# Optimization experiments

Measured on AMD Instinct MI355X. Metric: run time of the kernel, lower is better.

The kernel has to match this reference:

```python
import jax, jax.numpy as jnp
import numpy as np

N_A, N_B = 100000, 100000
N = N_A + N_B
E = 600000
D_IN_A, D_IN_B = 64, 96
HID, OUT = 128, 64
R, BASES = 4, 4


def setup_inputs() -> dict:
    key = jax.random.key(0)
    ks = jax.random.split(key, 16)
    inp = {
        "x_author": jax.random.normal(ks[0], (N_A, D_IN_A), jnp.float32),
        "x_paper": jax.random.normal(ks[1], (N_B, D_IN_B), jnp.float32),
        "src": jax.random.randint(ks[2], (E,), 0, N, jnp.int32),
        "dst": jax.random.randint(ks[3], (E,), 0, N, jnp.int32),
        "edge_type": jax.random.randint(ks[4], (E,), 0, R, jnp.int32),
        # per-node-type linear projections (with bias, as nn.Linear)
        "W_proj_a": jax.random.normal(ks[5], (D_IN_A, HID), jnp.float32) / np.sqrt(D_IN_A),
        "b_proj_a": jnp.zeros((HID,), jnp.float32),
        "W_proj_b": jax.random.normal(ks[6], (D_IN_B, HID), jnp.float32) / np.sqrt(D_IN_B),
        "b_proj_b": jnp.zeros((HID,), jnp.float32),
        # conv0: hid->hid, root_weight=False
        "basis0": jax.random.normal(ks[7], (BASES, HID, HID), jnp.float32) / np.sqrt(HID),
        "comp0": jax.random.normal(ks[8], (R, BASES), jnp.float32) / np.sqrt(BASES),
        # conv1: hid->hid, root_weight=True
        "basis1": jax.random.normal(ks[9], (BASES, HID, HID), jnp.float32) / np.sqrt(HID),
        "comp1": jax.random.normal(ks[10], (R, BASES), jnp.float32) / np.sqrt(BASES),
        "root1": jax.random.normal(ks[11], (HID, HID), jnp.float32) / np.sqrt(HID),
        # conv2: hid->out, root_weight=True
        "basis2": jax.random.normal(ks[12], (BASES, HID, OUT), jnp.float32) / np.sqrt(HID),
        "comp2": jax.random.normal(ks[13], (R, BASES), jnp.float32) / np.sqrt(BASES),
        "root2": jax.random.normal(ks[14], (HID, OUT), jnp.float32) / np.sqrt(HID),
    }
    return inp


def rgcn_conv(x, src, dst, etype, basis, comp, root):
    # basis-decomposed relation weights: [R, in, out]
    W = jnp.einsum('rb,bio->rio', comp, basis)
    out = jnp.zeros((x.shape[0], W.shape[2]), x.dtype)
    for r in range(R):  # small fixed relation count
        xw = x @ W[r]                                  # [N, out]
        m = (etype == r)
        msg = jnp.where(m[:, None], xw[src], 0.0)      # [E, out]
        s = jax.ops.segment_sum(msg, dst, num_segments=x.shape[0])
        cnt = jax.ops.segment_sum(m.astype(x.dtype), dst, num_segments=x.shape[0])
        out = out + s / jnp.maximum(cnt, 1.0)[:, None]  # per-relation mean aggr
    if root is not None:
        out = out + x @ root
    return out


def reference(x_author, x_paper, src, dst, edge_type,
              W_proj_a, b_proj_a, W_proj_b, b_proj_b,
              basis0, comp0, basis1, comp1, root1, basis2, comp2, root2):
    # per-node-type projection + relu, then concat in node_type order
    ha = jax.nn.relu(x_author @ W_proj_a + b_proj_a)
    hp = jax.nn.relu(x_paper @ W_proj_b + b_proj_b)
    x = jnp.concatenate([ha, hp], axis=0)             # [N, HID]
    x_lat0 = x
    # dropout skipped (eval mode)
    x = jax.nn.relu(rgcn_conv(x, src, dst, edge_type, basis0, comp0, None))
    x_lat1 = x
    x = jax.nn.relu(rgcn_conv(x, src, dst, edge_type, basis1, comp1, root1))
    x_lat2 = x
    x = rgcn_conv(x, src, dst, edge_type, basis2, comp2, root2)
    return (x, x_lat0, x_lat1, x_lat2)
```

## Files before the change

### kernel.cpp

```cpp
#include <hip/hip_runtime.h>

constexpr int NNODES = 200000;
constexpr int NAUT   = 100000;
constexpr int NEDGE  = 600000;
constexpr int HIDC   = 128;
constexpr int OUTCH  = 64;
constexpr int RELS   = 4;
constexpr int SCAN_N = RELS * NNODES;
constexpr int LDB    = HIDC + 8;

typedef __attribute__((ext_vector_type(8))) short bf16x8;
typedef __attribute__((ext_vector_type(4))) float f32x4;

__device__ __forceinline__ unsigned short f2bf(float f) {
    unsigned int b = __float_as_uint(f);
    b += 0x7FFFu + ((b >> 16) & 1u);
    return (unsigned short)(b >> 16);
}
__device__ __forceinline__ float bf2f(unsigned short u) {
    return __uint_as_float(((unsigned int)u) << 16);
}

__device__ __forceinline__ int fragoff(int k, int n, int NB) {
    return ((k >> 5) * NB + (n >> 4)) * 512 + (((k >> 3) & 3) * 16 + (n & 15)) * 8 + (k & 7);
}


__global__ void count_kernel(const int* __restrict__ dst, const int* __restrict__ et,
                             int* __restrict__ bins) {
    int e = blockIdx.x * 256 + threadIdx.x;
    if (e < NEDGE) atomicAdd(&bins[et[e] * NNODES + dst[e]], 1);
}

__global__ void scan_fused_kernel(int* __restrict__ bins, int* __restrict__ binCur,
                                  int* __restrict__ gctr) {
    __shared__ int s[256];
    __shared__ int sbase;
    int b = blockIdx.x, t = threadIdx.x;
    int base = b * 1024 + t * 4;
    int v[4], sum = 0;
#pragma unroll
    for (int i = 0; i < 4; i++) {
        v[i] = (base + i < SCAN_N) ? bins[base + i] : 0;
        sum += v[i];
    }
    s[t] = sum;
    __syncthreads();
    for (int off = 1; off < 256; off <<= 1) {
        int x = (t >= off) ? s[t - off] : 0;
        __syncthreads();
        if (t >= off) s[t] += x;
        __syncthreads();
    }
    if (t == 255) sbase = atomicAdd(gctr, s[255]);
    __syncthreads();
    int run = sbase + s[t] - sum;
#pragma unroll
    for (int i = 0; i < 4; i++) {
        if (base + i < SCAN_N) {
            bins[base + i] = run;
            binCur[base + i] = run;
        }
        run += v[i];
    }
}

__global__ void scatter_kernel(const int* __restrict__ src, const int* __restrict__ dst,
                               const int* __restrict__ et, int* __restrict__ binCur,
                               int* __restrict__ srcSorted) {
    int e = blockIdx.x * 256 + threadIdx.x;
    if (e < NEDGE) {
        int bin = et[e] * NNODES + dst[e];
        int pos = atomicAdd(&binCur[bin], 1);
        srcSorted[pos] = src[e];
    }
}

__global__ void fragify_kernel(const float* __restrict__ basis0, const float* __restrict__ comp0,
                               const float* __restrict__ basis1, const float* __restrict__ comp1,
                               const float* __restrict__ root1,
                               const float* __restrict__ basis2, const float* __restrict__ comp2,
                               const float* __restrict__ root2,
                               short* __restrict__ whi0, short* __restrict__ wlo0,
                               short* __restrict__ whi1, short* __restrict__ wlo1,
                               short* __restrict__ whiR1, short* __restrict__ wloR1,
                               short* __restrict__ whi2, short* __restrict__ wlo2,
                               short* __restrict__ whiR2, short* __restrict__ wloR2) {
    int idx = blockIdx.x * 256 + threadIdx.x;
    if (idx >= 188416) return;
    float w;
    short *hp, *lp;
    if (idx < 65536) {
        int r = idx >> 14, e = idx & 16383;
        int k = e >> 7, n = e & 127;
        w = 0.f;
#pragma unroll
        for (int b = 0; b < 4; b++) w += comp0[r * 4 + b] * basis0[b * 16384 + e];
        int off = r * 16384 + fragoff(k, n, 8);
        hp = whi0 + off; lp = wlo0 + off;
    } else if (idx < 131072) {
        int i2 = idx - 65536;
        int r = i2 >> 14, e = i2 & 16383;
        int k = e >> 7, n = e & 127;
        w = 0.f;
#pragma unroll
        for (int b = 0; b < 4; b++) w += comp1[r * 4 + b] * basis1[b * 16384 + e];
        int off = r * 16384 + fragoff(k, n, 8);
        hp = whi1 + off; lp = wlo1 + off;
    } else if (idx < 147456) {
        int e = idx - 131072;
        int k = e >> 7, n = e & 127;
        w = root1[e];
        int off = fragoff(k, n, 8);
        hp = whiR1 + off; lp = wloR1 + off;
    } else if (idx < 180224) {
        int i2 = idx - 147456;
        int r = i2 >> 13, e = i2 & 8191;
        int k = e >> 6, n = e & 63;
        w = 0.f;
#pragma unroll
        for (int b = 0; b < 4; b++) w += comp2[r * 4 + b] * basis2[b * 8192 + e];
        int off = r * 8192 + fragoff(k, n, 4);
        hp = whi2 + off; lp = wlo2 + off;
    } else {
        int e = idx - 180224;
        int k = e >> 6, n = e & 63;
        w = root2[e];
        int off = fragoff(k, n, 4);
        hp = whiR2 + off; lp = wloR2 + off;
    }
    unsigned short h = f2bf(w);
    unsigned short l = f2bf(w - bf2f(h));
    *hp = (short)h;
    *lp = (short)l;
}

__global__ __launch_bounds__(256) void gemm_kernel(const float* __restrict__ A,
                                                   const float* __restrict__ B,
                                                   const float* __restrict__ bias,
                                                   float* __restrict__ C, int M, int K) {
    __shared__ float sA[64 * 128];
    int tid = threadIdx.x;
    int row0 = blockIdx.x * 64;

    for (int i = tid; i < (64 * K) >> 2; i += 256) {
        int off = i << 2;
        int rr = off / K, cc = off % K;
        int row = row0 + rr;
        float4 v = {0.f, 0.f, 0.f, 0.f};
        if (row < M) v = *(const float4*)(A + (long)row * K + cc);
        *(float4*)(sA + rr * K + cc) = v;
    }
    __syncthreads();

    int cg = tid & 31, rg = tid >> 5;
    int c0 = cg * 4, r0 = rg * 8;
    float acc[8][4];
#pragma unroll
    for (int i = 0; i < 8; i++)
#pragma unroll
        for (int j = 0; j < 4; j++) acc[i][j] = 0.f;

#pragma unroll 2
    for (int k = 0; k < K; k += 4) {
        float a[8][4];
#pragma unroll
        for (int i = 0; i < 8; i++)
            *(float4*)(a[i]) = *(const float4*)(sA + (r0 + i) * K + k);
#pragma unroll
        for (int j = 0; j < 4; j++) {
            float b[4];
            *(float4*)b = *(const float4*)(B + (k + j) * 128 + c0);
#pragma unroll
            for (int i = 0; i < 8; i++)
#pragma unroll
                for (int jj = 0; jj < 4; jj++)
                    acc[i][jj] = fmaf(a[i][j], b[jj], acc[i][jj]);
        }
    }

#pragma unroll
    for (int i = 0; i < 8; i++) {
        int row = row0 + r0 + i;
        if (row >= M) continue;
        float v[4];
#pragma unroll
        for (int jj = 0; jj < 4; jj++) v[jj] = fmaxf(acc[i][jj] + bias[c0 + jj], 0.f);
        *(float4*)(C + (long)row * 128 + c0) = *(float4*)v;
    }
}

template <int NC, bool HASROOT, bool DORELU>
__global__ __launch_bounds__(512) void conv_kernel(const float* __restrict__ x,
                                                   const short* __restrict__ whiRel,
                                                   const short* __restrict__ wloRel,
                                                   const short* __restrict__ whiRoot,
                                                   const short* __restrict__ wloRoot,
                                                   const int* __restrict__ binStart,
                                                   const int* __restrict__ binEnd,
                                                   const int* __restrict__ srcSorted,
                                                   float* __restrict__ out) {
    constexpr int NB  = NC / 16;
    constexpr int KB  = HIDC / 32;
    constexpr int TPW = NB / 2;
    __shared__ short sHi[64 * LDB];
    __shared__ short sLo[64 * LDB];
    int tid = threadIdx.x;
    int v0 = blockIdx.x * 64;

    const int grow = tid >> 3, gq = tid & 7;
    const int wave = tid >> 6, lane = tid & 63;
    const int lrow = lane & 15, lgrp = lane >> 4;
    const int rt = wave >> 1, ch = wave & 1;

    f32x4 acc[TPW];
#pragma unroll
    for (int t = 0; t < TPW; t++) acc[t] = (f32x4){0.f, 0.f, 0.f, 0.f};

    constexpr int NPHASE = HASROOT ? RELS + 1 : RELS;
#pragma unroll 1
    for (int ph = 0; ph < NPHASE; ph++) {
        if (ph > 0) __syncthreads();
        if (ph < RELS) {
            int bin = ph * NNODES + v0 + grow;
            int s = binStart[bin], e = binEnd[bin];
            float4 a4[4];
#pragma unroll
            for (int i = 0; i < 4; i++) a4[i] = make_float4(0.f, 0.f, 0.f, 0.f);
            int j = s;
            int idx = (j < e) ? srcSorted[j] : 0;
            while (j < e) {
                int nidx = (j + 1 < e) ? srcSorted[j + 1] : 0;
                const float* xs = x + (long)idx * HIDC;
#pragma unroll
                for (int i = 0; i < 4; i++) {
                    float4 v = *(const float4*)(xs + (gq + i * 8) * 4);
                    a4[i].x += v.x; a4[i].y += v.y; a4[i].z += v.z; a4[i].w += v.w;
                }
                idx = nidx;
                ++j;
            }
            float sc = 1.0f / (float)max(e - s, 1);
#pragma unroll
            for (int i = 0; i < 4; i++) {
                float4 w = a4[i];
                w.x *= sc; w.y *= sc; w.z *= sc; w.w *= sc;
                unsigned short h0 = f2bf(w.x), h1 = f2bf(w.y), h2 = f2bf(w.z), h3 = f2bf(w.w);
                unsigned short l0 = f2bf(w.x - bf2f(h0)), l1 = f2bf(w.y - bf2f(h1));
                unsigned short l2 = f2bf(w.z - bf2f(h2)), l3 = f2bf(w.w - bf2f(h3));
                int c = (gq + i * 8) * 4;
                uint2 hv = make_uint2((unsigned)h0 | ((unsigned)h1 << 16),
                                      (unsigned)h2 | ((unsigned)h3 << 16));
                uint2 lv = make_uint2((unsigned)l0 | ((unsigned)l1 << 16),
                                      (unsigned)l2 | ((unsigned)l3 << 16));
                *(uint2*)(sHi + grow * LDB + c) = hv;
                *(uint2*)(sLo + grow * LDB + c) = lv;
            }
        } else {
#pragma unroll
            for (int i = 0; i < 4; i++) {
                int i4 = tid + 512 * i;
                int row = i4 >> 5, col4 = i4 & 31;
                float4 w = *(const float4*)(x + (long)(v0 + row) * HIDC + col4 * 4);
                unsigned short h0 = f2bf(w.x), h1 = f2bf(w.y), h2 = f2bf(w.z), h3 = f2bf(w.w);
                unsigned short l0 = f2bf(w.x - bf2f(h0)), l1 = f2bf(w.y - bf2f(h1));
                unsigned short l2 = f2bf(w.z - bf2f(h2)), l3 = f2bf(w.w - bf2f(h3));
                int c = col4 * 4;
                uint2 hv = make_uint2((unsigned)h0 | ((unsigned)h1 << 16),
                                      (unsigned)h2 | ((unsigned)h3 << 16));
                uint2 lv = make_uint2((unsigned)l0 | ((unsigned)l1 << 16),
                                      (unsigned)l2 | ((unsigned)l3 << 16));
                *(uint2*)(sHi + row * LDB + c) = hv;
                *(uint2*)(sLo + row * LDB + c) = lv;
            }
        }
        __syncthreads();

        const short* __restrict__ bhB = (ph < RELS) ? (whiRel + ph * (KB * NB * 512)) : whiRoot;
        const short* __restrict__ blB = (ph < RELS) ? (wloRel + ph * (KB * NB * 512)) : wloRoot;

#pragma unroll
        for (int kb = 0; kb < KB; kb++) {
            int aoff = (rt * 16 + lrow) * LDB + kb * 32 + lgrp * 8;
            bf16x8 ah = *(const bf16x8*)(sHi + aoff);
            bf16x8 al = *(const bf16x8*)(sLo + aoff);
#pragma unroll
            for (int t = 0; t < TPW; t++) {
                int nb = ch * TPW + t;
                int boff = ((kb * NB + nb) * 64 + lane) * 8;
                bf16x8 bh = *(const bf16x8*)(bhB + boff);
                bf16x8 bl = *(const bf16x8*)(blB + boff);
                acc[t] = __builtin_amdgcn_mfma_f32_16x16x32_bf16(ah, bh, acc[t], 0, 0, 0);
                acc[t] = __builtin_amdgcn_mfma_f32_16x16x32_bf16(al, bh, acc[t], 0, 0, 0);
                acc[t] = __builtin_amdgcn_mfma_f32_16x16x32_bf16(ah, bl, acc[t], 0, 0, 0);
            }
        }
    }

#pragma unroll
    for (int t = 0; t < TPW; t++) {
        int nb = ch * TPW + t;
        int col = nb * 16 + lrow;
#pragma unroll
        for (int j = 0; j < 4; j++) {
            float vv = acc[t][j];
            if (DORELU) vv = fmaxf(vv, 0.f);
            out[(long)(v0 + rt * 16 + lgrp * 4 + j) * NC + col] = vv;
        }
    }
}


extern "C" void kernel_launch(void* const* d_in, const int* in_sizes, int n_in,
                              void* d_out, int out_size, void* d_ws, size_t ws_size,
                              hipStream_t stream) {
    const float* xa     = (const float*)d_in[0];
    const float* xp     = (const float*)d_in[1];
    const int*   src    = (const int*)d_in[2];
    const int*   dst    = (const int*)d_in[3];
    const int*   et     = (const int*)d_in[4];
    const float* Wpa    = (const float*)d_in[5];
    const float* bpa    = (const float*)d_in[6];
    const float* Wpb    = (const float*)d_in[7];
    const float* bpb    = (const float*)d_in[8];
    const float* basis0 = (const float*)d_in[9];
    const float* comp0  = (const float*)d_in[10];
    const float* basis1 = (const float*)d_in[11];
    const float* comp1  = (const float*)d_in[12];
    const float* root1  = (const float*)d_in[13];
    const float* basis2 = (const float*)d_in[14];
    const float* comp2  = (const float*)d_in[15];
    const float* root2  = (const float*)d_in[16];

    float* out_final = (float*)d_out;
    float* x0 = out_final + (size_t)NNODES * OUTCH;
    float* x1 = x0 + (size_t)NNODES * HIDC;
    float* x2 = x1 + (size_t)NNODES * HIDC;

    int* bins      = (int*)d_ws;
    int* binCur    = bins + SCAN_N;
    int* gctr      = binCur + SCAN_N;
    int* srcSorted = gctr + 800;
    short* whi0  = (short*)(srcSorted + NEDGE);
    short* wlo0  = whi0 + 65536;
    short* whi1  = wlo0 + 65536;
    short* wlo1  = whi1 + 65536;
    short* whiR1 = wlo1 + 65536;
    short* wloR1 = whiR1 + 16384;
    short* whi2  = wloR1 + 16384;
    short* wlo2  = whi2 + 32768;
    short* whiR2 = wlo2 + 32768;
    short* wloR2 = whiR2 + 8192;

    dim3 b256(256);
    dim3 b512(512);
    int egrid = (NEDGE + 255) / 256;
    int nScanBlocks = (SCAN_N + 1023) / 1024;

    hipMemsetAsync(bins, 0, (size_t)SCAN_N * sizeof(int), stream);
    hipMemsetAsync(gctr, 0, sizeof(int), stream);
    hipLaunchKernelGGL(count_kernel, dim3(egrid), b256, 0, stream, dst, et, bins);
    hipLaunchKernelGGL(scan_fused_kernel, dim3(nScanBlocks), b256, 0, stream,
                       bins, binCur, gctr);
    hipLaunchKernelGGL(scatter_kernel, dim3(egrid), b256, 0, stream,
                       src, dst, et, binCur, srcSorted);

    hipLaunchKernelGGL(fragify_kernel, dim3((188416 + 255) / 256), b256, 0, stream,
                       basis0, comp0, basis1, comp1, root1, basis2, comp2, root2,
                       whi0, wlo0, whi1, wlo1, whiR1, wloR1, whi2, wlo2, whiR2, wloR2);

    hipLaunchKernelGGL(gemm_kernel, dim3((NAUT + 63) / 64), b256, 0, stream,
                       xa, Wpa, bpa, x0, NAUT, 64);
    hipLaunchKernelGGL(gemm_kernel, dim3((NAUT + 63) / 64), b256, 0, stream,
                       xp, Wpb, bpb, x0 + (size_t)NAUT * HIDC, NAUT, 96);

    int cgrid = NNODES / 64;

    hipLaunchKernelGGL((conv_kernel<128, false, true>), dim3(cgrid), b512, 0, stream,
                       x0, whi0, wlo0, (const short*)nullptr, (const short*)nullptr,
                       bins, binCur, srcSorted, x1);
    hipLaunchKernelGGL((conv_kernel<128, true, true>), dim3(cgrid), b512, 0, stream,
                       x1, whi1, wlo1, whiR1, wloR1, bins, binCur, srcSorted, x2);
    hipLaunchKernelGGL((conv_kernel<64, true, false>), dim3(cgrid), b512, 0, stream,
                       x2, whi2, wlo2, whiR2, wloR2, bins, binCur, srcSorted, out_final);
}
```

Before: 1.076 ms.

## Restructure conv kernel to 256 threads with wave-per-row gather and column-split MFMA

Cuts the conv block from 512 to 256 threads (4 waves). In the gather phase each wave now walks 16 destination rows one at a time, with all 64 lanes reading a float2 slice of each source row, instead of 8 threads per row reading float4. In the MFMA phase each wave owns a column slice and all 4 row tiles, so its B fragments load once per k-block and are reused across row tiles. This trades gather parallelism (serial row loops with dependent index loads) for fewer B loads and more accumulators per wave, which raises register pressure.

```diff
diff --git a/kernel.cpp b/kernel.cpp
--- a/kernel.cpp
+++ b/kernel.cpp
@@ -191,7 +191,7 @@
 }
 
 template <int NC, bool HASROOT, bool DORELU>
-__global__ __launch_bounds__(512) void conv_kernel(const float* __restrict__ x,
+__global__ __launch_bounds__(256) void conv_kernel(const float* __restrict__ x,
                                                    const short* __restrict__ whiRel,
                                                    const short* __restrict__ wloRel,
                                                    const short* __restrict__ whiRoot,
@@ -202,76 +202,59 @@
                                                    float* __restrict__ out) {
     constexpr int NB  = NC / 16;
     constexpr int KB  = HIDC / 32;
-    constexpr int TPW = NB / 2;
+    constexpr int TPW = NB / 4;
     __shared__ short sHi[64 * LDB];
     __shared__ short sLo[64 * LDB];
     int tid = threadIdx.x;
     int v0 = blockIdx.x * 64;
 
-    const int grow = tid >> 3, gq = tid & 7;
     const int wave = tid >> 6, lane = tid & 63;
     const int lrow = lane & 15, lgrp = lane >> 4;
-    const int rt = wave >> 1, ch = wave & 1;
-
-    f32x4 acc[TPW];
-#pragma unroll
-    for (int t = 0; t < TPW; t++) acc[t] = (f32x4){0.f, 0.f, 0.f, 0.f};
+    const int c2 = lane * 2;
+
+    f32x4 acc[4][TPW];
+#pragma unroll
+    for (int rt = 0; rt < 4; rt++)
+#pragma unroll
+        for (int t = 0; t < TPW; t++) acc[rt][t] = (f32x4){0.f, 0.f, 0.f, 0.f};
 
     constexpr int NPHASE = HASROOT ? RELS + 1 : RELS;
 #pragma unroll 1
     for (int ph = 0; ph < NPHASE; ph++) {
         if (ph > 0) __syncthreads();
         if (ph < RELS) {
-            int bin = ph * NNODES + v0 + grow;
-            int s = binStart[bin], e = binEnd[bin];
-            float4 a4[4];
-#pragma unroll
-            for (int i = 0; i < 4; i++) a4[i] = make_float4(0.f, 0.f, 0.f, 0.f);
-            int j = s;
-            int idx = (j < e) ? srcSorted[j] : 0;
-            while (j < e) {
-                int nidx = (j + 1 < e) ? srcSorted[j + 1] : 0;
-                const float* xs = x + (long)idx * HIDC;
-#pragma unroll
-                for (int i = 0; i < 4; i++) {
-                    float4 v = *(const float4*)(xs + (gq + i * 8) * 4);
-                    a4[i].x += v.x; a4[i].y += v.y; a4[i].z += v.z; a4[i].w += v.w;
+#pragma unroll 1
+            for (int rr = 0; rr < 16; rr++) {
+                int row = wave * 16 + rr;
+                int bin = ph * NNODES + v0 + row;
+                int s = binStart[bin], e = binEnd[bin];
+                float a0 = 0.f, a1 = 0.f;
+                int j = s;
+                int idx = (j < e) ? srcSorted[j] : 0;
+#pragma unroll 1
+                for (; j < e; j++) {
+                    int nidx = (j + 1 < e) ? srcSorted[j + 1] : 0;
+                    float2 u = *(const float2*)(x + (long)idx * HIDC + c2);
+                    a0 += u.x;
+                    a1 += u.y;
+                    idx = nidx;
                 }
-                idx = nidx;
-                ++j;
-            }
-            float sc = 1.0f / (float)max(e - s, 1);
-#pragma unroll
-            for (int i = 0; i < 4; i++) {
-                float4 w = a4[i];
-                w.x *= sc; w.y *= sc; w.z *= sc; w.w *= sc;
-                unsigned short h0 = f2bf(w.x), h1 = f2bf(w.y), h2 = f2bf(w.z), h3 = f2bf(w.w);
-                unsigned short l0 = f2bf(w.x - bf2f(h0)), l1 = f2bf(w.y - bf2f(h1));
-                unsigned short l2 = f2bf(w.z - bf2f(h2)), l3 = f2bf(w.w - bf2f(h3));
-                int c = (gq + i * 8) * 4;
-                uint2 hv = make_uint2((unsigned)h0 | ((unsigned)h1 << 16),
-                                      (unsigned)h2 | ((unsigned)h3 << 16));
-                uint2 lv = make_uint2((unsigned)l0 | ((unsigned)l1 << 16),
-                                      (unsigned)l2 | ((unsigned)l3 << 16));
-                *(uint2*)(sHi + grow * LDB + c) = hv;
-                *(uint2*)(sLo + grow * LDB + c) = lv;
+                float sc = 1.0f / (float)max(e - s, 1);
+                a0 *= sc; a1 *= sc;
+                unsigned short h0 = f2bf(a0), h1 = f2bf(a1);
+                unsigned short l0 = f2bf(a0 - bf2f(h0)), l1 = f2bf(a1 - bf2f(h1));
+                *(unsigned int*)(sHi + row * LDB + c2) = (unsigned)h0 | ((unsigned)h1 << 16);
+                *(unsigned int*)(sLo + row * LDB + c2) = (unsigned)l0 | ((unsigned)l1 << 16);
             }
         } else {
-#pragma unroll
-            for (int i = 0; i < 4; i++) {
-                int i4 = tid + 512 * i;
-                int row = i4 >> 5, col4 = i4 & 31;
-                float4 w = *(const float4*)(x + (long)(v0 + row) * HIDC + col4 * 4);
-                unsigned short h0 = f2bf(w.x), h1 = f2bf(w.y), h2 = f2bf(w.z), h3 = f2bf(w.w);
-                unsigned short l0 = f2bf(w.x - bf2f(h0)), l1 = f2bf(w.y - bf2f(h1));
-                unsigned short l2 = f2bf(w.z - bf2f(h2)), l3 = f2bf(w.w - bf2f(h3));
-                int c = col4 * 4;
-                uint2 hv = make_uint2((unsigned)h0 | ((unsigned)h1 << 16),
-                                      (unsigned)h2 | ((unsigned)h3 << 16));
-                uint2 lv = make_uint2((unsigned)l0 | ((unsigned)l1 << 16),
-                                      (unsigned)l2 | ((unsigned)l3 << 16));
-                *(uint2*)(sHi + row * LDB + c) = hv;
-                *(uint2*)(sLo + row * LDB + c) = lv;
+#pragma unroll 1
+            for (int rr = 0; rr < 16; rr++) {
+                int row = wave * 16 + rr;
+                float2 u = *(const float2*)(x + (long)(v0 + row) * HIDC + c2);
+                unsigned short h0 = f2bf(u.x), h1 = f2bf(u.y);
+                unsigned short l0 = f2bf(u.x - bf2f(h0)), l1 = f2bf(u.y - bf2f(h1));
+                *(unsigned int*)(sHi + row * LDB + c2) = (unsigned)h0 | ((unsigned)h1 << 16);
+                *(unsigned int*)(sLo + row * LDB + c2) = (unsigned)l0 | ((unsigned)l1 << 16);
             }
         }
         __syncthreads();
@@ -281,33 +264,42 @@
 
 #pragma unroll
         for (int kb = 0; kb < KB; kb++) {
-            int aoff = (rt * 16 + lrow) * LDB + kb * 32 + lgrp * 8;
-            bf16x8 ah = *(const bf16x8*)(sHi + aoff);
-            bf16x8 al = *(const bf16x8*)(sLo + aoff);
+            bf16x8 bh[TPW], bl[TPW];
 #pragma unroll
             for (int t = 0; t < TPW; t++) {
-                int nb = ch * TPW + t;
+                int nb = wave * TPW + t;
                 int boff = ((kb * NB + nb) * 64 + lane) * 8;
-                bf16x8 bh = *(const bf16x8*)(bhB + boff);
-                bf16x8 bl = *(const bf16x8*)(blB + boff);
-                acc[t] = __builtin_amdgcn_mfma_f32_16x16x32_bf16(ah, bh, acc[t], 0, 0, 0);
-                acc[t] = __builtin_amdgcn_mfma_f32_16x16x32_bf16(al, bh, acc[t], 0, 0, 0);
-                acc[t] = __builtin_amdgcn_mfma_f32_16x16x32_bf16(ah, bl, acc[t], 0, 0, 0);
-            }
-        }
-    }
-
-#pragma unroll
-    for (int t = 0; t < TPW; t++) {
-        int nb = ch * TPW + t;
-        int col = nb * 16 + lrow;
-#pragma unroll
-        for (int j = 0; j < 4; j++) {
-            float vv = acc[t][j];
-            if (DORELU) vv = fmaxf(vv, 0.f);
-            out[(long)(v0 + rt * 16 + lgrp * 4 + j) * NC + col] = vv;
-        }
-    }
+                bh[t] = *(const bf16x8*)(bhB + boff);
+                bl[t] = *(const bf16x8*)(blB + boff);
+            }
+#pragma unroll
+            for (int rt = 0; rt < 4; rt++) {
+                int aoff = (rt * 16 + lrow) * LDB + kb * 32 + lgrp * 8;
+                bf16x8 ah = *(const bf16x8*)(sHi + aoff);
+                bf16x8 al = *(const bf16x8*)(sLo + aoff);
+#pragma unroll
+                for (int t = 0; t < TPW; t++) {
+                    acc[rt][t] = __builtin_amdgcn_mfma_f32_16x16x32_bf16(ah, bh[t], acc[rt][t], 0, 0, 0);
+                    acc[rt][t] = __builtin_amdgcn_mfma_f32_16x16x32_bf16(al, bh[t], acc[rt][t], 0, 0, 0);
+                    acc[rt][t] = __builtin_amdgcn_mfma_f32_16x16x32_bf16(ah, bl[t], acc[rt][t], 0, 0, 0);
+                }
+            }
+        }
+    }
+
+#pragma unroll
+    for (int rt = 0; rt < 4; rt++)
+#pragma unroll
+        for (int t = 0; t < TPW; t++) {
+            int nb = wave * TPW + t;
+            int col = nb * 16 + lrow;
+#pragma unroll
+            for (int j = 0; j < 4; j++) {
+                float vv = acc[rt][t][j];
+                if (DORELU) vv = fmaxf(vv, 0.f);
+                out[(long)(v0 + rt * 16 + lgrp * 4 + j) * NC + col] = vv;
+            }
+        }
 }
 
 
@@ -353,7 +345,6 @@
     short* wloR2 = whiR2 + 8192;
 
     dim3 b256(256);
-    dim3 b512(512);
     int egrid = (NEDGE + 255) / 256;
     int nScanBlocks = (SCAN_N + 1023) / 1024;
 
@@ -376,11 +367,11 @@
 
     int cgrid = NNODES / 64;
 
-    hipLaunchKernelGGL((conv_kernel<128, false, true>), dim3(cgrid), b512, 0, stream,
+    hipLaunchKernelGGL((conv_kernel<128, false, true>), dim3(cgrid), b256, 0, stream,
                        x0, whi0, wlo0, (const short*)nullptr, (const short*)nullptr,
                        bins, binCur, srcSorted, x1);
-    hipLaunchKernelGGL((conv_kernel<128, true, true>), dim3(cgrid), b512, 0, stream,
+    hipLaunchKernelGGL((conv_kernel<128, true, true>), dim3(cgrid), b256, 0, stream,
                        x1, whi1, wlo1, whiR1, wloR1, bins, binCur, srcSorted, x2);
-    hipLaunchKernelGGL((conv_kernel<64, true, false>), dim3(cgrid), b512, 0, stream,
+    hipLaunchKernelGGL((conv_kernel<64, true, false>), dim3(cgrid), b256, 0, stream,
                        x2, whi2, wlo2, whiR2, wloR2, bins, binCur, srcSorted, out_final);
 }
```

After: 1.267 ms. 17.8% more time.
